# Performance work log

Hardware: AMD Instinct MI355X
Metric: run time of the kernel (lower is better)

The kernel has to match this reference:

```python
import jax, jax.numpy as jnp
import numpy as np

B, T, D = 2, 2048, 1024
H = 4
KD = int(D * 0.5)      # total key dim = 512
VD = int(D * 1.0)      # total value dim = 1024
DK, DV = KD // H, VD // H  # per-head: 128, 256
CHUNK = 64
LOW_RANK = 16          # gate_low_rank_dim
NORMALIZER = 16.0      # gate_logit_normalizer
EPS = 1e-6


def setup_inputs() -> dict:
    key = jax.random.key(0)
    ks = jax.random.split(key, 10)
    def w(k, shape):
        return jax.random.normal(k, shape, jnp.float32) / np.sqrt(shape[0]).astype(np.float32)
    return {
        "x": jax.random.normal(ks[0], (B, T, D), jnp.float32),
        "Wq": w(ks[1], (D, KD)),
        "Wk": w(ks[2], (D, KD)),
        "Wv": w(ks[3], (D, VD)),
        "Wg": w(ks[4], (D, VD)),          # output gate projection
        "Wgk1": w(ks[5], (D, LOW_RANK)),  # low-rank gate proj (no bias)
        "Wgk2": w(ks[6], (LOW_RANK, KD)),
        "bgk2": jax.random.normal(ks[7], (KD,), jnp.float32) * 0.1,
        "gnorm_w": jnp.ones((DV,), jnp.float32),  # FusedRMSNormSwishGate weight
        "Wo": w(ks[8], (VD, D)),
    }


def reference(x, Wq, Wk, Wv, Wg, Wgk1, Wgk2, bgk2, gnorm_w, Wo):
    scale = DK ** -0.5
    NC = T // CHUNK
    # [B,T,d] -> [NC,B,H,C,d_head]
    to_heads = lambda a, d: a.reshape(B, NC, CHUNK, H, d).transpose(1, 0, 3, 2, 4)
    q = to_heads(x @ Wq, DK)
    k = to_heads(x @ Wk, DK)
    v = to_heads(x @ Wv, DV)
    # per-key log decay gate: logsigmoid(low-rank proj) / normalizer
    gk = jax.nn.log_sigmoid((x @ Wgk1) @ Wgk2 + bgk2) / NORMALIZER
    G = jnp.cumsum(to_heads(gk, DK), axis=3)  # inclusive cumsum within chunk

    def chunk_step(S, inp):
        k_c, v_c, G_c = inp                       # [B,H,C,DK],[B,H,C,DV],[B,H,C,DK]
        G_last = G_c[:, :, -1, :]                 # [B,H,DK] total chunk decay
        k_bar = k_c * jnp.exp(G_last[:, :, None, :] - G_c)  # decay pos->chunk end
        S_new = jnp.exp(G_last)[..., None] * S + jnp.einsum('bhck,bhcv->bhkv', k_bar, v_c)
        return S_new, S                           # emit state at chunk START

    S0 = jnp.zeros((B, H, DK, DV), x.dtype)
    _, S_prev = jax.lax.scan(chunk_step, S0, (k, v, G))  # [NC,B,H,DK,DV]

    qg = q * jnp.exp(G) * scale                   # decay-scaled queries
    o_inter = jnp.einsum('nbhck,nbhkv->nbhcv', qg, S_prev)
    kg = k * jnp.exp(-G)
    A = jnp.einsum('nbhik,nbhjk->nbhij', qg, kg)  # intra-chunk scores
    A = jnp.where(jnp.tril(jnp.ones((CHUNK, CHUNK), bool)), A, 0.0)
    o = o_inter + jnp.einsum('nbhij,nbhjv->nbhiv', A, v)  # [NC,B,H,C,DV]
    o = o.transpose(1, 0, 3, 2, 4).reshape(B, T, H, DV)

    # fused gated RMSNorm: rmsnorm(o)*weight * swish(g), then output proj
    g = (x @ Wg).reshape(B, T, H, DV)
    o = o * jax.lax.rsqrt(jnp.mean(o * o, axis=-1, keepdims=True) + EPS) * gnorm_w
    o = o * (g * jax.nn.sigmoid(g))
    return o.reshape(B, T, VD) @ Wo
```

## Files before the change

### kernel.cpp

```cpp
#include <hip/hip_runtime.h>
#include <hip/hip_bf16.h>

#define BDIM 2
#define TDIM 2048
#define DDIM 1024
#define HH 4
#define KD 512
#define VD 1024
#define DK 128
#define DV 256
#define NC 32
#define CHUNKC 64
#define MTOT (BDIM*TDIM)
#define NALL 3584
#define STRIDE_ST ((size_t)BDIM*HH*DK*DV)

typedef __bf16 bf16x8 __attribute__((ext_vector_type(8)));
typedef float  f32x4  __attribute__((ext_vector_type(4)));
typedef __hip_bfloat16 hbf;

__device__ __forceinline__ void async_copy16(const void* g, void* l) {
  __builtin_amdgcn_global_load_lds(
      (const __attribute__((address_space(1))) void*)g,
      (__attribute__((address_space(3))) void*)l, 16, 0, 0);
}

__global__ void cast_bf16_kernel(const float* __restrict__ src, hbf* __restrict__ dst) {
  int t = blockIdx.x*256 + threadIdx.x;
  float4 v = ((const float4*)src)[t];
  union { hbf h[4]; uint2 u; } o;
  o.h[0] = __float2bfloat16(v.x); o.h[1] = __float2bfloat16(v.y);
  o.h[2] = __float2bfloat16(v.z); o.h[3] = __float2bfloat16(v.w);
  ((uint2*)dst)[t] = o.u;
}

__global__ void transpose_cast_kernel(const float* __restrict__ W, hbf* __restrict__ Wt,
                                      int K, int N) {
  __shared__ float tile[32][33];
  const int bx = blockIdx.x, by = blockIdx.y;
  const int tx = threadIdx.x & 31, ty = threadIdx.x >> 5;
  #pragma unroll
  for (int r = ty; r < 32; r += 8)
    tile[r][tx] = W[(size_t)(by*32 + r)*N + bx*32 + tx];
  __syncthreads();
  #pragma unroll
  for (int r = ty; r < 32; r += 8)
    Wt[(size_t)(bx*32 + r)*K + by*32 + tx] = __float2bfloat16(tile[tx][r]);
}

__global__ void wcomp_kernel(const float* __restrict__ W1, const float* __restrict__ W2,
                             hbf* __restrict__ Wct) {
  int idx = blockIdx.x*256 + threadIdx.x;
  int k = idx & 1023, n = idx >> 10;
  float s = 0.f;
  #pragma unroll
  for (int r = 0; r < 16; ++r) s += W1[k*16 + r] * W2[r*KD + n];
  Wct[(size_t)n*DDIM + k] = __float2bfloat16(s);
}

template <int MODE>
__global__ __launch_bounds__(256) void gemm_bt(const hbf* __restrict__ A,
                                               const hbf* __restrict__ Bt,
                                               float* __restrict__ Cf,
                                               hbf* __restrict__ Cq,
                                               hbf* __restrict__ Cv,
                                               int M, int N, int K) {
  __shared__ hbf As[128][32];
  __shared__ hbf Bs[128][32];
  const int t = threadIdx.x;
  const int w = t >> 6, l = t & 63;
  const int lr = l >> 2, lc = (l & 3)*8;
  const int lane16 = l & 15, quad = l >> 4;
  const int row0 = blockIdx.y*128, col0 = blockIdx.x*128;
  const int mb = (w >> 1)*64, nb = (w & 1)*64;

  const hbf* ga = A  + (size_t)(row0 + w*32 + lr)*K + lc;
  const hbf* gb = Bt + (size_t)(col0 + w*32 + lr)*K + lc;
  hbf* la0 = &As[w*32][0];      hbf* la1 = &As[w*32 + 16][0];
  hbf* lb0 = &Bs[w*32][0];      hbf* lb1 = &Bs[w*32 + 16][0];
  const size_t rstep = (size_t)16*K;

  f32x4 acc[4][4] = {};
  for (int k0 = 0; k0 < K; k0 += 32) {
    async_copy16(ga,         la0);
    async_copy16(ga + rstep, la1);
    async_copy16(gb,         lb0);
    async_copy16(gb + rstep, lb1);
    ga += 32; gb += 32;
    __syncthreads();
    bf16x8 af[4], bfr[4];
    #pragma unroll
    for (int i = 0; i < 4; ++i)
      af[i] = *(const bf16x8*)&As[mb + i*16 + lane16][quad*8];
    #pragma unroll
    for (int j = 0; j < 4; ++j)
      bfr[j] = *(const bf16x8*)&Bs[nb + j*16 + lane16][quad*8];
    #pragma unroll
    for (int i = 0; i < 4; ++i)
      #pragma unroll
      for (int j = 0; j < 4; ++j)
        acc[i][j] = __builtin_amdgcn_mfma_f32_16x16x32_bf16(af[i], bfr[j], acc[i][j], 0, 0, 0);
    __syncthreads();
  }
  #pragma unroll
  for (int i = 0; i < 4; ++i)
    #pragma unroll
    for (int j = 0; j < 4; ++j)
      #pragma unroll
      for (int r = 0; r < 4; ++r) {
        int m = row0 + mb + i*16 + quad*4 + r;
        int n = col0 + nb + j*16 + lane16;
        float v = acc[i][j][r];
        if (MODE == 0) {
          Cf[(size_t)m*N + n] = v;
        } else {
          if (col0 < 1024)       Cq[(size_t)m*1024 + n] = __float2bfloat16(v);
          else if (col0 < 1536)  Cf[(size_t)m*512  + n - 1024] = v;
          else                   Cv[(size_t)m*2048 + n - 1536] = __float2bfloat16(v);
        }
      }
}

__global__ __launch_bounds__(256) void gkcumsum_kernel(float* __restrict__ Gb,
                                                       const float* __restrict__ bias) {
  __shared__ float buf[CHUNKC][128];
  const int cs = blockIdx.x & 3;
  const int nc = (blockIdx.x >> 2) & 31;
  const int b  = blockIdx.x >> 7;
  const int t = threadIdx.x;
  const int bc = b*TDIM + nc*CHUNKC;
  const int col0 = cs*128;
  #pragma unroll
  for (int i = 0; i < 32; ++i) {
    int idx = t + 256*i;
    int c = idx >> 7, col = idx & 127;
    float s = Gb[(size_t)(bc + c)*KD + col0 + col] + bias[col0 + col];
    float ls = fminf(s, 0.f) - log1pf(expf(-fabsf(s)));
    buf[c][col] = ls * (1.0f/16.0f);
  }
  __syncthreads();
  if (t < 128) {
    float acc = 0.f;
    #pragma unroll
    for (int c = 0; c < CHUNKC; ++c) {
      acc += buf[c][t];
      buf[c][t] = acc;
    }
  }
  __syncthreads();
  #pragma unroll
  for (int i = 0; i < 32; ++i) {
    int idx = t + 256*i;
    int c = idx >> 7, col = idx & 127;
    Gb[(size_t)(bc + c)*KD + col0 + col] = buf[c][col];
  }
}

__global__ __launch_bounds__(256) void state_chunk_kernel(const hbf* __restrict__ qkbf,
                                                          const hbf* __restrict__ vgbf,
                                                          const float* __restrict__ Gb,
                                                          hbf* __restrict__ Ub,
                                                          float* __restrict__ dec) {
  const int bh = blockIdx.x & 7;
  const int nc = blockIdx.x >> 3;
  const int b = bh >> 2, h = bh & 3;
  const int t = threadIdx.x;
  const int w = t >> 6, l = t & 63;
  const int lane16 = l & 15, quad = l >> 4;
  __shared__ hbf kbarT[DK][72];
  __shared__ hbf vT[DV][72];
  __shared__ float glast[DK];
  const int bc = b*TDIM + nc*CHUNKC;
  if (t < DK) {
    float gl = Gb[(size_t)(bc + 63)*KD + h*DK + t];
    glast[t] = gl;
    dec[((size_t)nc*8 + bh)*DK + t] = expf(gl);
  }
  __syncthreads();
  #pragma unroll
  for (int i = 0; i < 32; ++i) {
    int idx = t + 256*i;
    int c = idx >> 7, kk = idx & 127;
    float g  = Gb[(size_t)(bc + c)*KD + h*DK + kk];
    float kv = __bfloat162float(qkbf[(size_t)(bc + c)*1024 + 512 + h*DK + kk]);
    kbarT[kk][c] = __float2bfloat16(kv * expf(glast[kk] - g));
  }
  #pragma unroll
  for (int i = 0; i < 64; ++i) {
    int idx = t + 256*i;
    int c = idx >> 8, col = idx & 255;
    vT[col][c] = vgbf[(size_t)(bc + c)*2048 + h*DV + col];
  }
  __syncthreads();
  f32x4 acc[4][8] = {};
  #pragma unroll
  for (int kc = 0; kc < 2; ++kc) {
    bf16x8 av[4], bk[8];
    #pragma unroll
    for (int i = 0; i < 4; ++i)
      av[i] = *(const bf16x8*)&vT[w*64 + i*16 + lane16][kc*32 + quad*8];
    #pragma unroll
    for (int j = 0; j < 8; ++j)
      bk[j] = *(const bf16x8*)&kbarT[j*16 + lane16][kc*32 + quad*8];
    #pragma unroll
    for (int i = 0; i < 4; ++i)
      #pragma unroll
      for (int j = 0; j < 8; ++j)
        acc[i][j] = __builtin_amdgcn_mfma_f32_16x16x32_bf16(av[i], bk[j], acc[i][j], 0, 0, 0);
  }
  hbf* ub = Ub + ((size_t)nc*8 + bh)*((size_t)DK*DV);
  #pragma unroll
  for (int i = 0; i < 4; ++i)
    #pragma unroll
    for (int j = 0; j < 8; ++j)
      #pragma unroll
      for (int r = 0; r < 4; ++r) {
        int v = w*64 + i*16 + quad*4 + r;
        int k = j*16 + lane16;
        ub[(size_t)v*DK + k] = __float2bfloat16(acc[i][j][r]);
      }
}

__global__ __launch_bounds__(256) void state_scan_kernel(const hbf* __restrict__ Ub,
                                                         const float* __restrict__ dec,
                                                         hbf* __restrict__ Spb) {
  const int p = blockIdx.x*256 + threadIdx.x;
  const size_t e = (size_t)p*2;
  const int k = (int)(e & 127);
  const int bh = (int)(e >> 15);
  float S0 = 0.f, S1 = 0.f;
  for (int nc = 0; nc < NC; ++nc) {
    const size_t off = (size_t)nc*STRIDE_ST + e;
    uint uu = *(const uint*)(Ub + off);
    hbf u0 = *(const hbf*)&uu;
    hbf u1 = *((const hbf*)&uu + 1);
    union { hbf h[2]; uint u; } ov;
    ov.h[0] = __float2bfloat16(S0); ov.h[1] = __float2bfloat16(S1);
    *(uint*)(Spb + off) = ov.u;
    float2 d = *(const float2*)(dec + ((size_t)nc*8 + bh)*DK + k);
    S0 = S0 * d.x + __bfloat162float(u0);
    S1 = S1 * d.y + __bfloat162float(u1);
  }
}

__global__ __launch_bounds__(256) void out_kernel(const hbf* __restrict__ qkbf,
                                                  const hbf* __restrict__ vgbf,
                                                  const float* __restrict__ Gb,
                                                  const hbf* __restrict__ Spb,
                                                  const float* __restrict__ gnw,
                                                  hbf* __restrict__ obf) {
  const int blk = blockIdx.x;
  const int h = blk & 3, b = (blk >> 2) & 1, nc = blk >> 3;
  const int t = threadIdx.x;
  const int w = t >> 6, l = t & 63;
  const int lane16 = l & 15, quad = l >> 4;

  __shared__ __align__(16) unsigned char smem[64768];
  hbf (*qgs)[136] = (hbf(*)[136])(smem);
  hbf (*Ald)[72]  = (hbf(*)[72]) (smem + 17408);
  hbf (*kgs)[136] = (hbf(*)[136])(smem + 26624);
  hbf (*vT)[72]   = (hbf(*)[72]) (smem + 26624);
  float* ssum     = (float*)     (smem + 63488);
  float* invb     = (float*)     (smem + 64512);

  const float scale = 0.088388347648318447f;
  const int bc = b*TDIM + nc*CHUNKC;

  #pragma unroll
  for (int i = 0; i < 32; ++i) {
    int idx = t + 256*i;
    int c = idx >> 7, kk = idx & 127;
    float g = Gb[(size_t)(bc + c)*KD + h*DK + kk];
    float qv = __bfloat162float(qkbf[(size_t)(bc + c)*1024 + h*DK + kk]);
    float kv = __bfloat162float(qkbf[(size_t)(bc + c)*1024 + 512 + h*DK + kk]);
    qgs[c][kk] = __float2bfloat16(qv * expf(g) * scale);
    kgs[c][kk] = __float2bfloat16(kv * expf(-g));
  }
  __syncthreads();

  f32x4 acc1[4] = {};
  #pragma unroll
  for (int kc = 0; kc < 4; ++kc) {
    bf16x8 af = *(const bf16x8*)&qgs[w*16 + lane16][kc*32 + quad*8];
    #pragma unroll
    for (int j = 0; j < 4; ++j) {
      bf16x8 bf = *(const bf16x8*)&kgs[j*16 + lane16][kc*32 + quad*8];
      acc1[j] = __builtin_amdgcn_mfma_f32_16x16x32_bf16(af, bf, acc1[j], 0, 0, 0);
    }
  }
  __syncthreads();

  #pragma unroll
  for (int j = 0; j < 4; ++j)
    #pragma unroll
    for (int r = 0; r < 4; ++r) {
      int cr = w*16 + quad*4 + r;
      int cc = j*16 + lane16;
      Ald[cr][cc] = __float2bfloat16(cc <= cr ? acc1[j][r] : 0.f);
    }
  #pragma unroll
  for (int i = 0; i < 64; ++i) {
    int e = t + 256*i;
    int c = e >> 8, col = e & 255;
    vT[col][c] = vgbf[(size_t)(bc + c)*2048 + h*DV + col];
  }
  __syncthreads();

  const hbf* SpB = Spb + ((size_t)nc*8 + (b*HH + h))*((size_t)DK*DV);
  f32x4 acc[4][4] = {};
  #pragma unroll
  for (int kc = 0; kc < 4; ++kc) {
    bf16x8 af[4], bs[4];
    #pragma unroll
    for (int i = 0; i < 4; ++i)
      af[i] = *(const bf16x8*)&qgs[i*16 + lane16][kc*32 + quad*8];
    #pragma unroll
    for (int j = 0; j < 4; ++j) {
      int n = w*64 + j*16 + lane16;
      bs[j] = *(const bf16x8*)(SpB + (size_t)n*DK + kc*32 + quad*8);
    }
    #pragma unroll
    for (int i = 0; i < 4; ++i)
      #pragma unroll
      for (int j = 0; j < 4; ++j)
        acc[i][j] = __builtin_amdgcn_mfma_f32_16x16x32_bf16(af[i], bs[j], acc[i][j], 0, 0, 0);
  }
  #pragma unroll
  for (int kc = 0; kc < 2; ++kc) {
    bf16x8 aa[4], bv[4];
    #pragma unroll
    for (int i = 0; i < 4; ++i)
      aa[i] = *(const bf16x8*)&Ald[i*16 + lane16][kc*32 + quad*8];
    #pragma unroll
    for (int j = 0; j < 4; ++j)
      bv[j] = *(const bf16x8*)&vT[w*64 + j*16 + lane16][kc*32 + quad*8];
    #pragma unroll
    for (int i = 0; i < 4; ++i)
      #pragma unroll
      for (int j = 0; j < 4; ++j)
        acc[i][j] = __builtin_amdgcn_mfma_f32_16x16x32_bf16(aa[i], bv[j], acc[i][j], 0, 0, 0);
  }

  #pragma unroll
  for (int i = 0; i < 4; ++i)
    #pragma unroll
    for (int r = 0; r < 4; ++r) {
      float s = 0.f;
      #pragma unroll
      for (int j = 0; j < 4; ++j) s += acc[i][j][r]*acc[i][j][r];
      s += __shfl_xor(s, 1); s += __shfl_xor(s, 2);
      s += __shfl_xor(s, 4); s += __shfl_xor(s, 8);
      if (lane16 == 0) ssum[(i*16 + quad*4 + r)*4 + w] = s;
    }
  __syncthreads();
  if (t < 64) {
    float tot = ssum[t*4] + ssum[t*4+1] + ssum[t*4+2] + ssum[t*4+3];
    invb[t] = rsqrtf(tot * (1.0f/DV) + 1e-6f);
  }
  __syncthreads();
  float gnwv[4];
  #pragma unroll
  for (int j = 0; j < 4; ++j) gnwv[j] = gnw[w*64 + j*16 + lane16];
  #pragma unroll
  for (int i = 0; i < 4; ++i)
    #pragma unroll
    for (int r = 0; r < 4; ++r) {
      int m = i*16 + quad*4 + r;
      float inv = invb[m];
      size_t grow_ = (size_t)(bc + m)*2048 + 1024 + h*DV + w*64;
      size_t orow_ = (size_t)(bc + m)*VD + h*DV + w*64;
      #pragma unroll
      for (int j = 0; j < 4; ++j) {
        float gv = __bfloat162float(vgbf[grow_ + j*16 + lane16]);
        float sig = 1.f / (1.f + expf(-gv));
        float val = acc[i][j][r] * inv * gnwv[j];
        obf[orow_ + j*16 + lane16] = __float2bfloat16(val * (gv * sig));
      }
    }
}

extern "C" void kernel_launch(void* const* d_in, const int* in_sizes, int n_in,
                              void* d_out, int out_size, void* d_ws, size_t ws_size,
                              hipStream_t stream) {
  const float* x    = (const float*)d_in[0];
  const float* Wq   = (const float*)d_in[1];
  const float* Wk   = (const float*)d_in[2];
  const float* Wv   = (const float*)d_in[3];
  const float* Wg   = (const float*)d_in[4];
  const float* Wgk1 = (const float*)d_in[5];
  const float* Wgk2 = (const float*)d_in[6];
  const float* bgk2 = (const float*)d_in[7];
  const float* gnw  = (const float*)d_in[8];
  const float* Wo   = (const float*)d_in[9];
  float* out = (float*)d_out;

  float* ws  = (float*)d_ws;
  float* Gb  = ws;
  float* dec = Gb  + (size_t)MTOT*KD;
  hbf* xbf   = (hbf*)(dec + (size_t)NC*BDIM*HH*DK);
  hbf* wtall = xbf   + (size_t)MTOT*DDIM;
  hbf* wto   = wtall + (size_t)NALL*DDIM;
  hbf* qkbf  = wto   + (size_t)DDIM*DDIM;
  hbf* vgbf  = qkbf  + (size_t)MTOT*1024;
  hbf* Ub    = vgbf  + (size_t)MTOT*2048;
  hbf* Spb   = Ub    + (size_t)NC*STRIDE_ST;
  hbf* obf   = Ub;

  cast_bf16_kernel<<<MTOT*DDIM/4/256, 256, 0, stream>>>(x, xbf);
  transpose_cast_kernel<<<dim3(512/32, DDIM/32), 256, 0, stream>>>(Wq, wtall, DDIM, 512);
  transpose_cast_kernel<<<dim3(512/32, DDIM/32), 256, 0, stream>>>(Wk, wtall + (size_t)512*DDIM, DDIM, 512);
  wcomp_kernel<<<512*1024/256, 256, 0, stream>>>(Wgk1, Wgk2, wtall + (size_t)1024*DDIM);
  transpose_cast_kernel<<<dim3(1024/32, DDIM/32), 256, 0, stream>>>(Wv, wtall + (size_t)1536*DDIM, DDIM, 1024);
  transpose_cast_kernel<<<dim3(1024/32, DDIM/32), 256, 0, stream>>>(Wg, wtall + (size_t)2560*DDIM, DDIM, 1024);
  transpose_cast_kernel<<<dim3(1024/32, DDIM/32), 256, 0, stream>>>(Wo, wto, DDIM, 1024);

  gemm_bt<1><<<dim3(NALL/128, MTOT/128), 256, 0, stream>>>(xbf, wtall, Gb, qkbf, vgbf, MTOT, NALL, DDIM);

  gkcumsum_kernel<<<256, 256, 0, stream>>>(Gb, bgk2);
  state_chunk_kernel<<<NC*BDIM*HH, 256, 0, stream>>>(qkbf, vgbf, Gb, Ub, dec);
  state_scan_kernel<<<(int)(STRIDE_ST/2/256), 256, 0, stream>>>(Ub, dec, Spb);
  out_kernel<<<NC*BDIM*HH, 256, 0, stream>>>(qkbf, vgbf, Gb, Spb, gnw, obf);
  gemm_bt<0><<<dim3(DDIM/128, MTOT/128), 256, 0, stream>>>(obf, wto, out, (hbf*)nullptr, (hbf*)nullptr, MTOT, DDIM, DDIM);
}
```

Baseline: 254.6 us.

## Merge weight prep launches into one kernel and double GEMM K-step

Six separate weight transpose/cast and low-rank gate composition launches become a single kernel, with each block choosing its source matrix by column range. This removes per-launch overhead and lets the small kernels run concurrently. The GEMM now loads two 32-wide K slices per iteration into separate LDS buffers, which halves the number of barrier pairs and doubles the loads in flight, at the cost of twice the shared memory.

```diff
diff --git a/kernel.cpp b/kernel.cpp
--- a/kernel.cpp
+++ b/kernel.cpp
@@ -34,28 +34,38 @@
   ((uint2*)dst)[t] = o.u;
 }
 
-__global__ void transpose_cast_kernel(const float* __restrict__ W, hbf* __restrict__ Wt,
-                                      int K, int N) {
+__global__ void prep_weights(const float* __restrict__ Wq, const float* __restrict__ Wk,
+                             const float* __restrict__ Wv, const float* __restrict__ Wg,
+                             const float* __restrict__ Wo, const float* __restrict__ W1,
+                             const float* __restrict__ W2,
+                             hbf* __restrict__ wtall, hbf* __restrict__ wto) {
   __shared__ float tile[32][33];
-  const int bx = blockIdx.x, by = blockIdx.y;
+  const int n0 = blockIdx.x*32, k0 = blockIdx.y*32;
   const int tx = threadIdx.x & 31, ty = threadIdx.x >> 5;
+  if (n0 >= 1024 && n0 < 1536) {
+    #pragma unroll
+    for (int r = ty; r < 32; r += 8) {
+      int n = n0 - 1024 + r, k = k0 + tx;
+      float s = 0.f;
+      #pragma unroll
+      for (int j = 0; j < 16; ++j) s += W1[(size_t)k*16 + j] * W2[(size_t)j*KD + n];
+      wtall[(size_t)(n0 + r)*DDIM + k] = __float2bfloat16(s);
+    }
+    return;
+  }
+  const float* W; int Nsrc, nloc; hbf* outp; int orow;
+  if      (n0 < 512)  { W = Wq; Nsrc = 512;  nloc = n0;        outp = wtall; orow = n0; }
+  else if (n0 < 1024) { W = Wk; Nsrc = 512;  nloc = n0 - 512;  outp = wtall; orow = n0; }
+  else if (n0 < 2560) { W = Wv; Nsrc = 1024; nloc = n0 - 1536; outp = wtall; orow = n0; }
+  else if (n0 < 3584) { W = Wg; Nsrc = 1024; nloc = n0 - 2560; outp = wtall; orow = n0; }
+  else                { W = Wo; Nsrc = 1024; nloc = n0 - 3584; outp = wto;   orow = n0 - 3584; }
   #pragma unroll
   for (int r = ty; r < 32; r += 8)
-    tile[r][tx] = W[(size_t)(by*32 + r)*N + bx*32 + tx];
+    tile[r][tx] = W[(size_t)(k0 + r)*Nsrc + nloc + tx];
   __syncthreads();
   #pragma unroll
   for (int r = ty; r < 32; r += 8)
-    Wt[(size_t)(bx*32 + r)*K + by*32 + tx] = __float2bfloat16(tile[tx][r]);
-}
-
-__global__ void wcomp_kernel(const float* __restrict__ W1, const float* __restrict__ W2,
-                             hbf* __restrict__ Wct) {
-  int idx = blockIdx.x*256 + threadIdx.x;
-  int k = idx & 1023, n = idx >> 10;
-  float s = 0.f;
-  #pragma unroll
-  for (int r = 0; r < 16; ++r) s += W1[k*16 + r] * W2[r*KD + n];
-  Wct[(size_t)n*DDIM + k] = __float2bfloat16(s);
+    outp[(size_t)(orow + r)*DDIM + k0 + tx] = __float2bfloat16(tile[tx][r]);
 }
 
 template <int MODE>
@@ -65,8 +75,8 @@
                                                hbf* __restrict__ Cq,
                                                hbf* __restrict__ Cv,
                                                int M, int N, int K) {
-  __shared__ hbf As[128][32];
-  __shared__ hbf Bs[128][32];
+  __shared__ hbf As0[128][32], As1[128][32];
+  __shared__ hbf Bs0[128][32], Bs1[128][32];
   const int t = threadIdx.x;
   const int w = t >> 6, l = t & 63;
   const int lr = l >> 2, lc = (l & 3)*8;
@@ -76,30 +86,52 @@
 
   const hbf* ga = A  + (size_t)(row0 + w*32 + lr)*K + lc;
   const hbf* gb = Bt + (size_t)(col0 + w*32 + lr)*K + lc;
-  hbf* la0 = &As[w*32][0];      hbf* la1 = &As[w*32 + 16][0];
-  hbf* lb0 = &Bs[w*32][0];      hbf* lb1 = &Bs[w*32 + 16][0];
+  hbf* la0 = &As0[w*32][0];   hbf* la1 = &As0[w*32 + 16][0];
+  hbf* la2 = &As1[w*32][0];   hbf* la3 = &As1[w*32 + 16][0];
+  hbf* lb0 = &Bs0[w*32][0];   hbf* lb1 = &Bs0[w*32 + 16][0];
+  hbf* lb2 = &Bs1[w*32][0];   hbf* lb3 = &Bs1[w*32 + 16][0];
   const size_t rstep = (size_t)16*K;
 
   f32x4 acc[4][4] = {};
-  for (int k0 = 0; k0 < K; k0 += 32) {
-    async_copy16(ga,         la0);
-    async_copy16(ga + rstep, la1);
-    async_copy16(gb,         lb0);
-    async_copy16(gb + rstep, lb1);
-    ga += 32; gb += 32;
+  for (int k0 = 0; k0 < K; k0 += 64) {
+    async_copy16(ga,              la0);
+    async_copy16(ga + rstep,      la1);
+    async_copy16(ga + 32,         la2);
+    async_copy16(ga + rstep + 32, la3);
+    async_copy16(gb,              lb0);
+    async_copy16(gb + rstep,      lb1);
+    async_copy16(gb + 32,         lb2);
+    async_copy16(gb + rstep + 32, lb3);
+    ga += 64; gb += 64;
     __syncthreads();
-    bf16x8 af[4], bfr[4];
-    #pragma unroll
-    for (int i = 0; i < 4; ++i)
-      af[i] = *(const bf16x8*)&As[mb + i*16 + lane16][quad*8];
-    #pragma unroll
-    for (int j = 0; j < 4; ++j)
-      bfr[j] = *(const bf16x8*)&Bs[nb + j*16 + lane16][quad*8];
-    #pragma unroll
-    for (int i = 0; i < 4; ++i)
+    {
+      bf16x8 af[4], bfr[4];
+      #pragma unroll
+      for (int i = 0; i < 4; ++i)
+        af[i] = *(const bf16x8*)&As0[mb + i*16 + lane16][quad*8];
       #pragma unroll
       for (int j = 0; j < 4; ++j)
-        acc[i][j] = __builtin_amdgcn_mfma_f32_16x16x32_bf16(af[i], bfr[j], acc[i][j], 0, 0, 0);
+        bfr[j] = *(const bf16x8*)&Bs0[nb + j*16 + lane16][quad*8];
+      #pragma unroll
+      for (int i = 0; i < 4; ++i)
+        #pragma unroll
+        for (int j = 0; j < 4; ++j)
+          acc[i][j] = __builtin_amdgcn_mfma_f32_16x16x32_bf16(af[i], bfr[j], acc[i][j], 0, 0, 0);
+    }
+    {
+      bf16x8 af[4], bfr[4];
+      #pragma unroll
+      for (int i = 0; i < 4; ++i)
+        af[i] = *(const bf16x8*)&As1[mb + i*16 + lane16][quad*8];
+      #pragma unroll
+      for (int j = 0; j < 4; ++j)
+        bfr[j] = *(const bf16x8*)&Bs1[nb + j*16 + lane16][quad*8];
+      #pragma unroll
+      for (int i = 0; i < 4; ++i)
+        #pragma unroll
+        for (int j = 0; j < 4; ++j)
+          acc[i][j] = __builtin_amdgcn_mfma_f32_16x16x32_bf16(af[i], bfr[j], acc[i][j], 0, 0, 0);
+    }
     __syncthreads();
   }
   #pragma unroll
@@ -407,12 +439,7 @@
   hbf* obf   = Ub;
 
   cast_bf16_kernel<<<MTOT*DDIM/4/256, 256, 0, stream>>>(x, xbf);
-  transpose_cast_kernel<<<dim3(512/32, DDIM/32), 256, 0, stream>>>(Wq, wtall, DDIM, 512);
-  transpose_cast_kernel<<<dim3(512/32, DDIM/32), 256, 0, stream>>>(Wk, wtall + (size_t)512*DDIM, DDIM, 512);
-  wcomp_kernel<<<512*1024/256, 256, 0, stream>>>(Wgk1, Wgk2, wtall + (size_t)1024*DDIM);
-  transpose_cast_kernel<<<dim3(1024/32, DDIM/32), 256, 0, stream>>>(Wv, wtall + (size_t)1536*DDIM, DDIM, 1024);
-  transpose_cast_kernel<<<dim3(1024/32, DDIM/32), 256, 0, stream>>>(Wg, wtall + (size_t)2560*DDIM, DDIM, 1024);
-  transpose_cast_kernel<<<dim3(1024/32, DDIM/32), 256, 0, stream>>>(Wo, wto, DDIM, 1024);
+  prep_weights<<<dim3(144, 32), 256, 0, stream>>>(Wq, Wk, Wv, Wg, Wo, Wgk1, Wgk2, wtall, wto);
 
   gemm_bt<1><<<dim3(NALL/128, MTOT/128), 256, 0, stream>>>(xbf, wtall, Gb, qkbf, vgbf, MTOT, NALL, DDIM);
 
```

Measured after the change: 230.3 us. -9.6%, faster.
